# Performance work log

Hardware: AMD Instinct MI355X
Metric: run time of the kernel (lower is better)

## Reference

```python
import jax, jax.numpy as jnp
import numpy as np

B, N, D = 16, 2048, 128

def setup_inputs() -> dict:
    key = jax.random.key(0)
    kq, kk, kv = jax.random.split(key, 3)
    q = jax.random.normal(kq, (B, N, D), dtype=jnp.float32)
    k = jax.random.normal(kk, (B, N, D), dtype=jnp.float32)
    v = jax.random.normal(kv, (B, N, D), dtype=jnp.float32)
    return {"q": q, "k": k, "v": v}

def reference(q, k, v):
    # attn = softmax(q @ k^T, axis=2)   (NOTE: no temperature scaling, matching source)
    scores = jnp.einsum("bnd,bmd->bnm", q, k)  # [B, N, N]
    attn = jax.nn.softmax(scores, axis=2)
    # dropout p=0.0 -> identity
    output = jnp.einsum("bnm,bmd->bnd", attn, v)  # [B, N, D]
    return (output, attn)
```

## Files before the change

### kernel.cpp

```cpp
#include <hip/hip_runtime.h>

#define N 2048
#define D 128
#define BB 16

typedef __attribute__((ext_vector_type(8))) short s16x8;
typedef __attribute__((ext_vector_type(4))) float f32x4;

__device__ __forceinline__ void split2(float x0, float x1, unsigned& h, unsigned& l) {
    unsigned b0 = __float_as_uint(x0), b1 = __float_as_uint(x1);
    float r0 = x0 - __uint_as_float(b0 & 0xffff0000u);
    float r1 = x1 - __uint_as_float(b1 & 0xffff0000u);
    h = (b0 >> 16) | (b1 & 0xffff0000u);
    l = (__float_as_uint(r0) >> 16) | (__float_as_uint(r1) & 0xffff0000u);
}

__device__ __forceinline__ s16x8 pack16(uint4 u) {
    union { uint4 a; s16x8 b; } x; x.a = u; return x.b;
}

__global__ __launch_bounds__(256) void zero_kernel(float4* __restrict__ p, int n4) {
    int i = blockIdx.x * 256 + threadIdx.x;
    const int stride = gridDim.x * 256;
    for (; i < n4; i += stride) p[i] = make_float4(0.f, 0.f, 0.f, 0.f);
}

__global__ __launch_bounds__(256) void vt_kernel(const float* __restrict__ v,
                                                 unsigned short* __restrict__ vth,
                                                 unsigned short* __restrict__ vtl) {
    const int t    = threadIdx.x;
    const int lane = t & 63;
    const int w    = t >> 6;
    const int b    = blockIdx.z;
    const int n0   = blockIdx.x * 32 + w * 8;
    const int d    = blockIdx.y * 64 + lane;
    const float* vp = v + ((size_t)b * N + n0) * D + d;
    float x[8];
    #pragma unroll
    for (int i = 0; i < 8; ++i) x[i] = vp[(size_t)i * D];
    uint4 h, l;
    split2(x[0], x[1], h.x, l.x);
    split2(x[2], x[3], h.y, l.y);
    split2(x[4], x[5], h.z, l.z);
    split2(x[6], x[7], h.w, l.w);
    size_t idx = ((size_t)b * D + d) * N + n0;
    *(uint4*)(vth + idx) = h;
    *(uint4*)(vtl + idx) = l;
}

__global__ __launch_bounds__(256, 2) void qs_kernel(const float* __restrict__ q,
                                                    const float* __restrict__ k,
                                                    float* __restrict__ outp) {
    __shared__ unsigned short Qh[64 * 128], Ql[64 * 128];
    __shared__ unsigned short Kh[64 * 128], Kl[64 * 128];
    const int t = threadIdx.x, lane = t & 63, w = t >> 6;
    const int b = blockIdx.y, ib = blockIdx.x * 64;
    const int l15 = lane & 15, l4 = lane >> 4;
    const float* qp = q + ((size_t)b * N + ib) * D;
    const float* kp = k + (size_t)b * N * D;

    #pragma unroll
    for (int c = 0; c < 8; ++c) {
        int flat4 = c * 256 + t;
        int row = flat4 >> 5, f4 = flat4 & 31;
        float4 qv = *(const float4*)(qp + (size_t)row * D + f4 * 4);
        uint2 hh, ll;
        split2(qv.x, qv.y, hh.x, ll.x);
        split2(qv.z, qv.w, hh.y, ll.y);
        int idx = row * 128 + (((f4 >> 1) ^ (row & 7)) * 8) + (f4 & 1) * 4;
        *(uint2*)(Qh + idx) = hh;
        *(uint2*)(Ql + idx) = ll;
    }
    __syncthreads();
    s16x8 qh[4], ql[4];
    {
        int row = w * 16 + l15;
        #pragma unroll
        for (int ks = 0; ks < 4; ++ks) {
            int idx = row * 128 + (((ks * 4 + l4) ^ (row & 7)) * 8);
            qh[ks] = *(const s16x8*)(Qh + idx);
            ql[ks] = *(const s16x8*)(Ql + idx);
        }
    }

    float rs[4] = {0.f, 0.f, 0.f, 0.f};

    float4 kf[8];
    #pragma unroll
    for (int c = 0; c < 8; ++c) {
        int flat4 = c * 256 + t;
        int row = flat4 >> 5, f4 = flat4 & 31;
        kf[c] = *(const float4*)(kp + (size_t)row * D + f4 * 4);
    }

    for (int jc = 0; jc < 32; ++jc) {
        __syncthreads();
        #pragma unroll
        for (int c = 0; c < 8; ++c) {
            int flat4 = c * 256 + t;
            int row = flat4 >> 5, f4 = flat4 & 31;
            uint2 hh, ll;
            split2(kf[c].x, kf[c].y, hh.x, ll.x);
            split2(kf[c].z, kf[c].w, hh.y, ll.y);
            int idx = row * 128 + (((f4 >> 1) ^ (row & 7)) * 8) + (f4 & 1) * 4;
            *(uint2*)(Kh + idx) = hh;
            *(uint2*)(Kl + idx) = ll;
        }
        __syncthreads();
        if (jc < 31) {
            #pragma unroll
            for (int c = 0; c < 8; ++c) {
                int flat4 = c * 256 + t;
                int row = flat4 >> 5, f4 = flat4 & 31;
                kf[c] = *(const float4*)(kp + (size_t)((jc + 1) * 64 + row) * D + f4 * 4);
            }
        }
        f32x4 sacc[4] = {};
        #pragma unroll
        for (int ks = 0; ks < 4; ++ks) {
            s16x8 bh[4], bl[4];
            #pragma unroll
            for (int tj = 0; tj < 4; ++tj) {
                int row = tj * 16 + l15;
                int idx = row * 128 + (((ks * 4 + l4) ^ (row & 7)) * 8);
                bh[tj] = *(const s16x8*)(Kh + idx);
                bl[tj] = *(const s16x8*)(Kl + idx);
            }
            #pragma unroll
            for (int tj = 0; tj < 4; ++tj) {
                sacc[tj] = __builtin_amdgcn_mfma_f32_16x16x32_bf16(qh[ks], bh[tj], sacc[tj], 0, 0, 0);
                sacc[tj] = __builtin_amdgcn_mfma_f32_16x16x32_bf16(qh[ks], bl[tj], sacc[tj], 0, 0, 0);
                sacc[tj] = __builtin_amdgcn_mfma_f32_16x16x32_bf16(ql[ks], bh[tj], sacc[tj], 0, 0, 0);
            }
        }
        #pragma unroll
        for (int r = 0; r < 4; ++r)
            #pragma unroll
            for (int tj = 0; tj < 4; ++tj) rs[r] += __expf(sacc[tj][r]);
    }

    #pragma unroll
    for (int r = 0; r < 4; ++r) {
        float v0 = rs[r];
        v0 += __shfl_xor(v0, 1);
        v0 += __shfl_xor(v0, 2);
        v0 += __shfl_xor(v0, 4);
        v0 += __shfl_xor(v0, 8);
        if (l15 == 0)
            outp[((size_t)b * N + ib + w * 16 + l4 * 4 + r) * D] = v0;
    }
}

__global__ __launch_bounds__(256, 2) void fused_kernel(const float* __restrict__ q,
                                                       const float* __restrict__ k,
                                                       const unsigned short* __restrict__ vth,
                                                       const unsigned short* __restrict__ vtl,
                                                       float* __restrict__ attn,
                                                       float* __restrict__ outp) {
    __shared__ unsigned short Kh[64 * 128], Kl[64 * 128];
    __shared__ unsigned short Vh[128 * 64], Vl[128 * 64];
    float* Pf = (float*)Kh;

    const int t = threadIdx.x, lane = t & 63, w = t >> 6;
    const int b = blockIdx.y, ib = blockIdx.x * 64;
    const int l15 = lane & 15, l4 = lane >> 4;
    const float* qp = q + ((size_t)b * N + ib) * D;
    const float* kp = k + (size_t)b * N * D;
    const unsigned short* vhp = vth + (size_t)b * D * N;
    const unsigned short* vlp = vtl + (size_t)b * D * N;
    float* ap = attn + ((size_t)b * N + ib) * N;
    float* op = outp + ((size_t)b * N + ib) * D;

    float inv[4];
    #pragma unroll
    for (int r = 0; r < 4; ++r)
        inv[r] = 1.0f / op[(size_t)(w * 16 + l4 * 4 + r) * D];

    s16x8 qh[4], ql[4];
    {
        const float* qrow = qp + (size_t)(w * 16 + l15) * D;
        #pragma unroll
        for (int ks = 0; ks < 4; ++ks) {
            float4 x0 = *(const float4*)(qrow + ks * 32 + l4 * 8);
            float4 x1 = *(const float4*)(qrow + ks * 32 + l4 * 8 + 4);
            uint4 h, l;
            split2(x0.x, x0.y, h.x, l.x);
            split2(x0.z, x0.w, h.y, l.y);
            split2(x1.x, x1.y, h.z, l.z);
            split2(x1.z, x1.w, h.w, l.w);
            qh[ks] = pack16(h);
            ql[ks] = pack16(l);
        }
    }

    f32x4 oacc[8] = {};

    float4 kf[8];
    uint4 fh[4], fl[4];
    #pragma unroll
    for (int c = 0; c < 8; ++c) {
        int flat4 = c * 256 + t;
        int row = flat4 >> 5, f4 = flat4 & 31;
        kf[c] = *(const float4*)(kp + (size_t)row * D + f4 * 4);
    }
    #pragma unroll
    for (int c = 0; c < 4; ++c) {
        int flat = c * 256 + t;
        int d = flat >> 3, g = flat & 7;
        fh[c] = *(const uint4*)(vhp + (size_t)d * N + g * 8);
        fl[c] = *(const uint4*)(vlp + (size_t)d * N + g * 8);
    }

    for (int jc = 0; jc < 32; ++jc) {
        __syncthreads();
        #pragma unroll
        for (int c = 0; c < 8; ++c) {
            int flat4 = c * 256 + t;
            int row = flat4 >> 5, f4 = flat4 & 31;
            uint2 hh, ll;
            split2(kf[c].x, kf[c].y, hh.x, ll.x);
            split2(kf[c].z, kf[c].w, hh.y, ll.y);
            int idx = row * 128 + (((f4 >> 1) ^ (row & 7)) * 8) + (f4 & 1) * 4;
            *(uint2*)(Kh + idx) = hh;
            *(uint2*)(Kl + idx) = ll;
        }
        #pragma unroll
        for (int c = 0; c < 4; ++c) {
            int flat = c * 256 + t;
            int d = flat >> 3, g = flat & 7;
            int idx = d * 64 + ((g ^ (d & 7)) * 8);
            *(uint4*)(Vh + idx) = fh[c];
            *(uint4*)(Vl + idx) = fl[c];
        }
        __syncthreads();
        if (jc < 31) {
            #pragma unroll
            for (int c = 0; c < 8; ++c) {
                int flat4 = c * 256 + t;
                int row = flat4 >> 5, f4 = flat4 & 31;
                kf[c] = *(const float4*)(kp + (size_t)((jc + 1) * 64 + row) * D + f4 * 4);
            }
            #pragma unroll
            for (int c = 0; c < 4; ++c) {
                int flat = c * 256 + t;
                int d = flat >> 3, g = flat & 7;
                fh[c] = *(const uint4*)(vhp + (size_t)d * N + (jc + 1) * 64 + g * 8);
                fl[c] = *(const uint4*)(vlp + (size_t)d * N + (jc + 1) * 64 + g * 8);
            }
        }
        f32x4 sacc[4] = {};
        #pragma unroll
        for (int ks = 0; ks < 4; ++ks) {
            s16x8 bh[4], bl[4];
            #pragma unroll
            for (int tj = 0; tj < 4; ++tj) {
                int row = tj * 16 + l15;
                int idx = row * 128 + (((ks * 4 + l4) ^ (row & 7)) * 8);
                bh[tj] = *(const s16x8*)(Kh + idx);
                bl[tj] = *(const s16x8*)(Kl + idx);
            }
            #pragma unroll
            for (int tj = 0; tj < 4; ++tj) {
                sacc[tj] = __builtin_amdgcn_mfma_f32_16x16x32_bf16(qh[ks], bh[tj], sacc[tj], 0, 0, 0);
                sacc[tj] = __builtin_amdgcn_mfma_f32_16x16x32_bf16(qh[ks], bl[tj], sacc[tj], 0, 0, 0);
                sacc[tj] = __builtin_amdgcn_mfma_f32_16x16x32_bf16(ql[ks], bh[tj], sacc[tj], 0, 0, 0);
            }
        }
        __syncthreads();
        float* pw = Pf + w * (16 * 64);
        #pragma unroll
        for (int r = 0; r < 4; ++r) {
            int row = l4 * 4 + r;
            #pragma unroll
            for (int tj = 0; tj < 4; ++tj) {
                float pv = __expf(sacc[tj][r]) * inv[r];
                int gw = (tj * 4 + (l15 >> 2)) ^ ((row & 7) << 1);
                pw[row * 64 + gw * 4 + (l15 & 3)] = pv;
            }
        }
        #pragma unroll
        for (int m = 0; m < 4; ++m) {
            int row = (m & 1) * 8 + (lane >> 3);
            int lg  = (lane & 7) + (m >> 1) * 8;
            int pg  = lg ^ ((row & 7) << 1);
            float4 pv4 = *(const float4*)(pw + row * 64 + pg * 4);
            *(float4*)(ap + (size_t)(w * 16 + row) * N + jc * 64 + lg * 4) = pv4;
        }
        #pragma unroll
        for (int ks2 = 0; ks2 < 2; ++ks2) {
            int g0 = (ks2 * 8 + l4 * 2) ^ ((l15 & 7) << 1);
            float4 p0 = *(const float4*)(pw + l15 * 64 + g0 * 4);
            float4 p1 = *(const float4*)(pw + l15 * 64 + g0 * 4 + 4);
            uint4 h, l;
            split2(p0.x, p0.y, h.x, l.x);
            split2(p0.z, p0.w, h.y, l.y);
            split2(p1.x, p1.y, h.z, l.z);
            split2(p1.z, p1.w, h.w, l.w);
            s16x8 pah = pack16(h), pal = pack16(l);
            #pragma unroll
            for (int df = 0; df < 8; ++df) {
                int dr = df * 16 + l15;
                int idx = dr * 64 + (((ks2 * 4 + l4) ^ (dr & 7)) * 8);
                s16x8 vbh = *(const s16x8*)(Vh + idx);
                s16x8 vbl = *(const s16x8*)(Vl + idx);
                oacc[df] = __builtin_amdgcn_mfma_f32_16x16x32_bf16(pah, vbh, oacc[df], 0, 0, 0);
                oacc[df] = __builtin_amdgcn_mfma_f32_16x16x32_bf16(pah, vbl, oacc[df], 0, 0, 0);
                oacc[df] = __builtin_amdgcn_mfma_f32_16x16x32_bf16(pal, vbh, oacc[df], 0, 0, 0);
            }
        }
    }

    #pragma unroll
    for (int r = 0; r < 4; ++r) {
        int row = w * 16 + l4 * 4 + r;
        #pragma unroll
        for (int df = 0; df < 8; ++df)
            op[(size_t)row * D + df * 16 + l15] = oacc[df][r];
    }
}

__global__ __launch_bounds__(256) void qk_kernel(const float* __restrict__ q,
                                                 const float* __restrict__ k,
                                                 float* __restrict__ attn,
                                                 float* __restrict__ outp) {
    __shared__ unsigned short Qh[128 * 32], Ql[128 * 32];
    __shared__ unsigned short Kh[128 * 32], Kl[128 * 32];
    const int t  = threadIdx.x;
    const int b  = blockIdx.z;
    const int ib = blockIdx.y * 128;
    const int jb = blockIdx.x * 128;
    const float* qp = q + ((size_t)b * N + ib) * D;
    const float* kp = k + ((size_t)b * N + jb) * D;

    const int lane = t & 63;
    const int w    = t >> 6;
    const int wr   = (w >> 1) * 64;
    const int wc   = (w & 1) * 64;
    const int l15  = lane & 15;
    const int l4   = lane >> 4;

    f32x4 acc[4][4] = {};

    for (int ks = 0; ks < 4; ++ks) {
        __syncthreads();
        #pragma unroll
        for (int c = 0; c < 4; ++c) {
            int flat = c * 256 + t;
            int row  = flat >> 3;
            int f4   = flat & 7;
            float4 qv = *(const float4*)(qp + (size_t)row * D + ks * 32 + f4 * 4);
            float4 kv = *(const float4*)(kp + (size_t)row * D + ks * 32 + f4 * 4);
            int idx = row * 32 + (((f4 >> 1) ^ (row & 3)) * 8) + (f4 & 1) * 4;
            uint2 hh, ll;
            split2(qv.x, qv.y, hh.x, ll.x);
            split2(qv.z, qv.w, hh.y, ll.y);
            *(uint2*)(Qh + idx) = hh;
            *(uint2*)(Ql + idx) = ll;
            split2(kv.x, kv.y, hh.x, ll.x);
            split2(kv.z, kv.w, hh.y, ll.y);
            *(uint2*)(Kh + idx) = hh;
            *(uint2*)(Kl + idx) = ll;
        }
        __syncthreads();

        s16x8 ah[4], al[4], bh[4], bl[4];
        #pragma unroll
        for (int ti = 0; ti < 4; ++ti) {
            int row = wr + ti * 16 + l15;
            int idx = row * 32 + ((l4 ^ (row & 3)) * 8);
            ah[ti] = *(const s16x8*)(Qh + idx);
            al[ti] = *(const s16x8*)(Ql + idx);
        }
        #pragma unroll
        for (int tj = 0; tj < 4; ++tj) {
            int row = wc + tj * 16 + l15;
            int idx = row * 32 + ((l4 ^ (row & 3)) * 8);
            bh[tj] = *(const s16x8*)(Kh + idx);
            bl[tj] = *(const s16x8*)(Kl + idx);
        }
        #pragma unroll
        for (int ti = 0; ti < 4; ++ti)
            #pragma unroll
            for (int tj = 0; tj < 4; ++tj) {
                acc[ti][tj] = __builtin_amdgcn_mfma_f32_16x16x32_bf16(ah[ti], bh[tj], acc[ti][tj], 0, 0, 0);
                acc[ti][tj] = __builtin_amdgcn_mfma_f32_16x16x32_bf16(ah[ti], bl[tj], acc[ti][tj], 0, 0, 0);
                acc[ti][tj] = __builtin_amdgcn_mfma_f32_16x16x32_bf16(al[ti], bh[tj], acc[ti][tj], 0, 0, 0);
            }
    }

    #pragma unroll
    for (int ti = 0; ti < 4; ++ti) {
        #pragma unroll
        for (int r = 0; r < 4; ++r) {
            int row = ib + wr + ti * 16 + l4 * 4 + r;
            float* arow = attn + ((size_t)b * N + row) * N + jb + wc;
            float rs = 0.f;
            #pragma unroll
            for (int tj = 0; tj < 4; ++tj) {
                float e = __expf(acc[ti][tj][r]);
                arow[tj * 16 + l15] = e;
                rs += e;
            }
            rs += __shfl_xor(rs, 1);
            rs += __shfl_xor(rs, 2);
            rs += __shfl_xor(rs, 4);
            rs += __shfl_xor(rs, 8);
            if (l15 == 0) atomicAdd(outp + ((size_t)b * N + row) * D, rs);
        }
    }
}

__global__ __launch_bounds__(256) void pv_fb_kernel(const float* __restrict__ v,
                                                    float* __restrict__ attn,
                                                    float* __restrict__ outp) {
    __shared__ unsigned short Ph[64 * 64], Pl[64 * 64];
    __shared__ unsigned short Vth[128 * 64], Vtl[128 * 64];
    __shared__ float invs[64];
    const int t  = threadIdx.x;
    const int b  = blockIdx.y;
    const int ib = blockIdx.x * 64;
    float* ap       = attn + ((size_t)b * N + ib) * N;
    const float* vp = v + (size_t)b * N * D;
    float* op       = outp + ((size_t)b * N + ib) * D;

    if (t < 64) invs[t] = 1.0f / op[(size_t)t * D];

    const int lane = t & 63;
    const int w    = t >> 6;
    const int rg   = (w >> 1) * 32;
    const int dg   = (w & 1) * 64;
    const int l15  = lane & 15;
    const int l4   = lane >> 4;

    f32x4 acc[2][4] = {};

    float4 pe[4], va[4], vb[4];
    #pragma unroll
    for (int c = 0; c < 4; ++c) {
        int flat = c * 256 + t;
        pe[c] = *(const float4*)(ap + (size_t)(flat >> 4) * N + (flat & 15) * 4);
        int jp = flat >> 5, d4 = flat & 31;
        va[c] = *(const float4*)(vp + (size_t)(jp * 2) * D + d4 * 4);
        vb[c] = *(const float4*)(vp + (size_t)(jp * 2 + 1) * D + d4 * 4);
    }

    for (int jc = 0; jc < 32; ++jc) {
        __syncthreads();
        #pragma unroll
        for (int c = 0; c < 4; ++c) {
            int flat = c * 256 + t;
            int row = flat >> 4, j4 = flat & 15;
            float iv = invs[row];
            float4 p4;
            p4.x = pe[c].x * iv; p4.y = pe[c].y * iv;
            p4.z = pe[c].z * iv; p4.w = pe[c].w * iv;
            *(float4*)(ap + (size_t)row * N + jc * 64 + j4 * 4) = p4;
            uint2 hh, ll;
            split2(p4.x, p4.y, hh.x, ll.x);
            split2(p4.z, p4.w, hh.y, ll.y);
            int idx = row * 64 + (((j4 >> 1) ^ (row & 7)) * 8) + (j4 & 1) * 4;
            *(uint2*)(Ph + idx) = hh;
            *(uint2*)(Pl + idx) = ll;
        }
        #pragma unroll
        for (int c = 0; c < 4; ++c) {
            int flat = c * 256 + t;
            int jp = flat >> 5, d4 = flat & 31;
            int j = jp * 2;
            float4 v0 = va[c], v1 = vb[c];
            #pragma unroll
            for (int e = 0; e < 4; ++e) {
                float x0 = (&v0.x)[e], x1 = (&v1.x)[e];
                unsigned h, l;
                split2(x0, x1, h, l);
                int d = d4 * 4 + e;
                int idx = d * 64 + (((j >> 3) ^ (d & 7)) * 8) + (j & 7);
                *(unsigned*)(Vth + idx) = h;
                *(unsigned*)(Vtl + idx) = l;
            }
        }
        __syncthreads();
        if (jc < 31) {
            #pragma unroll
            for (int c = 0; c < 4; ++c) {
                int flat = c * 256 + t;
                pe[c] = *(const float4*)(ap + (size_t)(flat >> 4) * N + (jc + 1) * 64 + (flat & 15) * 4);
                int jp = flat >> 5, d4 = flat & 31;
                va[c] = *(const float4*)(vp + (size_t)((jc + 1) * 64 + jp * 2) * D + d4 * 4);
                vb[c] = *(const float4*)(vp + (size_t)((jc + 1) * 64 + jp * 2 + 1) * D + d4 * 4);
            }
        }
        #pragma unroll
        for (int ksj = 0; ksj < 2; ++ksj) {
            s16x8 pah[2], pal[2], bh[4], bl[4];
            #pragma unroll
            for (int ti = 0; ti < 2; ++ti) {
                int row = rg + ti * 16 + l15;
                int idx = row * 64 + (((ksj * 4 + l4) ^ (row & 7)) * 8);
                pah[ti] = *(const s16x8*)(Ph + idx);
                pal[ti] = *(const s16x8*)(Pl + idx);
            }
            #pragma unroll
            for (int tj = 0; tj < 4; ++tj) {
                int d = dg + tj * 16 + l15;
                int idx = d * 64 + (((ksj * 4 + l4) ^ (d & 7)) * 8);
                bh[tj] = *(const s16x8*)(Vth + idx);
                bl[tj] = *(const s16x8*)(Vtl + idx);
            }
            #pragma unroll
            for (int ti = 0; ti < 2; ++ti)
                #pragma unroll
                for (int tj = 0; tj < 4; ++tj) {
                    acc[ti][tj] = __builtin_amdgcn_mfma_f32_16x16x32_bf16(pah[ti], bh[tj], acc[ti][tj], 0, 0, 0);
                    acc[ti][tj] = __builtin_amdgcn_mfma_f32_16x16x32_bf16(pah[ti], bl[tj], acc[ti][tj], 0, 0, 0);
                    acc[ti][tj] = __builtin_amdgcn_mfma_f32_16x16x32_bf16(pal[ti], bh[tj], acc[ti][tj], 0, 0, 0);
                }
        }
    }

    #pragma unroll
    for (int ti = 0; ti < 2; ++ti)
        #pragma unroll
        for (int r = 0; r < 4; ++r) {
            int row = rg + ti * 16 + l4 * 4 + r;
            #pragma unroll
            for (int tj = 0; tj < 4; ++tj)
                op[(size_t)row * D + dg + tj * 16 + l15] = acc[ti][tj][r];
        }
}

extern "C" void kernel_launch(void* const* d_in, const int* in_sizes, int n_in,
                              void* d_out, int out_size, void* d_ws, size_t ws_size,
                              hipStream_t stream) {
    const float* q = (const float*)d_in[0];
    const float* k = (const float*)d_in[1];
    const float* v = (const float*)d_in[2];
    float* out  = (float*)d_out;
    float* attn = out + (size_t)BB * N * D;

    const size_t vt_elems = (size_t)BB * D * N;
    const bool use_ws = ws_size >= vt_elems * 2 * sizeof(unsigned short);

    if (use_ws) {
        unsigned short* vth = (unsigned short*)d_ws;
        unsigned short* vtl = vth + vt_elems;
        vt_kernel<<<dim3(N / 32, 2, BB), 256, 0, stream>>>(v, vth, vtl);
        qs_kernel<<<dim3(N / 64, BB), 256, 0, stream>>>(q, k, out);
        fused_kernel<<<dim3(N / 64, BB), 256, 0, stream>>>(q, k, vth, vtl, attn, out);
    } else {
        zero_kernel<<<1024, 256, 0, stream>>>((float4*)out, BB * N * D / 4);
        qk_kernel<<<dim3(N / 128, N / 128, BB), 256, 0, stream>>>(q, k, attn, out);
        pv_fb_kernel<<<dim3(N / 64, BB), 256, 0, stream>>>(v, attn, out);
    }
}
```

Measured before the change: 514.8 us.

## Swizzle block order for XCD locality, pad P tile, use nontemporal output stores

Switches qs and fused kernels to a 1D grid and remaps block indices so the 8 consecutive blocks that round-robin across XCDs land on the same batch, keeping each batch's K and V in one L2. It also pads the per-warp probability scratch rows to 68 floats to cut LDS bank conflicts, and writes the large attn matrix and the output with nontemporal stores to avoid polluting cache. The padding enlarges the P scratch, which must still fit inside the aliased K buffer.

```diff
diff --git a/kernel.cpp b/kernel.cpp
--- a/kernel.cpp
+++ b/kernel.cpp
@@ -3,6 +3,7 @@
 #define N 2048
 #define D 128
 #define BB 16
+#define PFS 68
 
 typedef __attribute__((ext_vector_type(8))) short s16x8;
 typedef __attribute__((ext_vector_type(4))) float f32x4;
@@ -54,7 +55,8 @@
     __shared__ unsigned short Qh[64 * 128], Ql[64 * 128];
     __shared__ unsigned short Kh[64 * 128], Kl[64 * 128];
     const int t = threadIdx.x, lane = t & 63, w = t >> 6;
-    const int b = blockIdx.y, ib = blockIdx.x * 64;
+    const int swz = (blockIdx.x & 7) * 64 + (blockIdx.x >> 3);
+    const int b = swz >> 5, ib = (swz & 31) * 64;
     const int l15 = lane & 15, l4 = lane >> 4;
     const float* qp = q + ((size_t)b * N + ib) * D;
     const float* kp = k + (size_t)b * N * D;
@@ -157,12 +159,15 @@
                                                        const unsigned short* __restrict__ vtl,
                                                        float* __restrict__ attn,
                                                        float* __restrict__ outp) {
-    __shared__ unsigned short Kh[64 * 128], Kl[64 * 128];
+    __shared__ unsigned short KBuf[2 * 64 * 128];
     __shared__ unsigned short Vh[128 * 64], Vl[128 * 64];
-    float* Pf = (float*)Kh;
+    unsigned short* Kh = KBuf;
+    unsigned short* Kl = KBuf + 64 * 128;
+    float* Pf = (float*)KBuf;
 
     const int t = threadIdx.x, lane = t & 63, w = t >> 6;
-    const int b = blockIdx.y, ib = blockIdx.x * 64;
+    const int swz = (blockIdx.x & 7) * 64 + (blockIdx.x >> 3);
+    const int b = swz >> 5, ib = (swz & 31) * 64;
     const int l15 = lane & 15, l4 = lane >> 4;
     const float* qp = q + ((size_t)b * N + ib) * D;
     const float* kp = k + (size_t)b * N * D;
@@ -267,7 +272,7 @@
             }
         }
         __syncthreads();
-        float* pw = Pf + w * (16 * 64);
+        float* pw = Pf + w * (16 * PFS);
         #pragma unroll
         for (int r = 0; r < 4; ++r) {
             int row = l4 * 4 + r;
@@ -275,7 +280,7 @@
             for (int tj = 0; tj < 4; ++tj) {
                 float pv = __expf(sacc[tj][r]) * inv[r];
                 int gw = (tj * 4 + (l15 >> 2)) ^ ((row & 7) << 1);
-                pw[row * 64 + gw * 4 + (l15 & 3)] = pv;
+                pw[row * PFS + gw * 4 + (l15 & 3)] = pv;
             }
         }
         #pragma unroll
@@ -283,14 +288,15 @@
             int row = (m & 1) * 8 + (lane >> 3);
             int lg  = (lane & 7) + (m >> 1) * 8;
             int pg  = lg ^ ((row & 7) << 1);
-            float4 pv4 = *(const float4*)(pw + row * 64 + pg * 4);
-            *(float4*)(ap + (size_t)(w * 16 + row) * N + jc * 64 + lg * 4) = pv4;
+            f32x4 pv4 = *(const f32x4*)(pw + row * PFS + pg * 4);
+            __builtin_nontemporal_store(pv4,
+                (f32x4*)(ap + (size_t)(w * 16 + row) * N + jc * 64 + lg * 4));
         }
         #pragma unroll
         for (int ks2 = 0; ks2 < 2; ++ks2) {
             int g0 = (ks2 * 8 + l4 * 2) ^ ((l15 & 7) << 1);
-            float4 p0 = *(const float4*)(pw + l15 * 64 + g0 * 4);
-            float4 p1 = *(const float4*)(pw + l15 * 64 + g0 * 4 + 4);
+            float4 p0 = *(const float4*)(pw + l15 * PFS + g0 * 4);
+            float4 p1 = *(const float4*)(pw + l15 * PFS + g0 * 4 + 4);
             uint4 h, l;
             split2(p0.x, p0.y, h.x, l.x);
             split2(p0.z, p0.w, h.y, l.y);
@@ -315,7 +321,8 @@
         int row = w * 16 + l4 * 4 + r;
         #pragma unroll
         for (int df = 0; df < 8; ++df)
-            op[(size_t)row * D + df * 16 + l15] = oacc[df][r];
+            __builtin_nontemporal_store(oacc[df][r],
+                op + (size_t)row * D + df * 16 + l15);
     }
 }
 
@@ -545,8 +552,8 @@
         unsigned short* vth = (unsigned short*)d_ws;
         unsigned short* vtl = vth + vt_elems;
         vt_kernel<<<dim3(N / 32, 2, BB), 256, 0, stream>>>(v, vth, vtl);
-        qs_kernel<<<dim3(N / 64, BB), 256, 0, stream>>>(q, k, out);
-        fused_kernel<<<dim3(N / 64, BB), 256, 0, stream>>>(q, k, vth, vtl, attn, out);
+        qs_kernel<<<(N / 64) * BB, 256, 0, stream>>>(q, k, out);
+        fused_kernel<<<(N / 64) * BB, 256, 0, stream>>>(q, k, vth, vtl, attn, out);
     } else {
         zero_kernel<<<1024, 256, 0, stream>>>((float4*)out, BB * N * D / 4);
         qk_kernel<<<dim3(N / 128, N / 128, BB), 256, 0, stream>>>(q, k, attn, out);
```

New measurement: 494.1 us. 4.0% less time.
